# Kernel tuning notes

Hardware: AMD Instinct MI355X
Metric: run time of the kernel (lower is better)

Reference implementation:

```python
import jax, jax.numpy as jnp
import numpy as np

B, G, K = 16, 5000, 256
NUM_CELLS, HID = 100, 64
STEPS, ALPHA = 10, 0.1


def setup_inputs() -> dict:
    key = jax.random.key(0)
    ks = jax.random.split(key, 10)
    ctl = jax.random.normal(ks[0], (B, G), dtype=jnp.float32)
    drug_targets = jax.random.uniform(ks[1], (B, G), dtype=jnp.float32)
    cell_idx = jax.random.randint(ks[2], (B,), 0, NUM_CELLS)
    drug_fp = jax.random.normal(ks[3], (B, 128), dtype=jnp.float32)
    # gene->module membership matrix (constructor constant M_gk)
    M = jax.random.uniform(ks[4], (G, K), dtype=jnp.float32)
    # module-module adjacency (constructor constant A_kk), column-normalized for stability
    A = jax.random.uniform(ks[5], (K, K), dtype=jnp.float32)
    A = A / jnp.sum(A, axis=0, keepdims=True)
    # shared Dense(hidden_dim, relu): input feature dim is 3 (ctl, t, z_gene stacked)
    W1 = jax.random.normal(ks[6], (3, HID), dtype=jnp.float32) * 0.5
    b1 = jnp.zeros((HID,), dtype=jnp.float32)
    cell_emb = jax.random.normal(ks[7], (NUM_CELLS, HID), dtype=jnp.float32) * 0.05
    W2 = jax.random.normal(ks[8], (HID, 1), dtype=jnp.float32) * 0.1
    b2 = jnp.zeros((1,), dtype=jnp.float32)
    return {"ctl": ctl, "drug_targets": drug_targets, "cell_idx": cell_idx,
            "drug_fp": drug_fp, "M": M, "A": A, "W1": W1, "b1": b1,
            "cell_emb": cell_emb, "W2": W2, "b2": b2}


def reference(ctl, drug_targets, cell_idx, drug_fp, M, A, W1, b1, cell_emb, W2, b2):
    t = drug_targets                                   # [B, G]
    # max-pool gene targets into modules: max_g t[b,g] * M[g,k]
    t_mod = jnp.max(t[:, :, None] * M[None, :, :], axis=1)   # [B, K]
    # APPNP propagation: Z = (1-alpha) * Z @ A + alpha * S, fixed 10 steps
    Z = t_mod
    for _ in range(STEPS):
        Z = (1.0 - ALPHA) * (Z @ A) + ALPHA * t_mod
    z_gene = Z @ M.T                                   # [B, G]
    x = jnp.stack([ctl, t, z_gene], axis=-1)           # [B, G, 3]
    h = jax.nn.relu(x @ W1 + b1)                       # [B, G, HID]
    h = h + cell_emb[cell_idx][:, None, :]             # broadcast cell embedding
    y = jnp.squeeze(h @ W2 + b2, axis=-1)              # [B, G]
    return y
```

## Files before the change

kernel.cpp:

```cpp
#include <hip/hip_runtime.h>

#define G 5000
#define K 256
#define BATCH 16
#define HID 64
#define STEPS 10
#define NC 125
#define GPER 40

__global__ void maxpool_kernel(const float* __restrict__ t,
                               const float* __restrict__ M,
                               const float* __restrict__ A,
                               float* __restrict__ partials,
                               float* __restrict__ awarm) {
    __shared__ float tl[GPER][BATCH];
    const int c  = blockIdx.x;
    const int k  = threadIdx.x;
    const int g0 = c * GPER;

    float4 aw = make_float4(0.f, 0.f, 0.f, 0.f);
    if (k < 128)
        aw = ((const float4*)A)[((size_t)blockIdx.x * 128 + k) & 16383];

    for (int i = k; i < GPER * BATCH; i += 256) {
        int gi = i >> 4, b = i & 15;
        tl[gi][b] = t[b * G + g0 + gi];
    }
    __syncthreads();

    float mx[BATCH];
#pragma unroll
    for (int b = 0; b < BATCH; ++b) mx[b] = 0.f;

#pragma unroll 4
    for (int gi = 0; gi < GPER; ++gi) {
        float mg = M[(size_t)(g0 + gi) * K + k];
#pragma unroll
        for (int b = 0; b < BATCH; ++b)
            mx[b] = fmaxf(mx[b], tl[gi][b] * mg);
    }
#pragma unroll
    for (int b = 0; b < BATCH; ++b)
        partials[((size_t)c * BATCH + b) * K + k] = mx[b];

    if (k < 128) awarm[k & 63] = aw.x + aw.y + aw.z + aw.w;
}

__global__ __launch_bounds__(1024, 4)
void appnp_fused(const float* __restrict__ partials,
                 const float* __restrict__ A,
                 const int* __restrict__ cell_idx,
                 const float* __restrict__ cell_emb,
                 const float* __restrict__ W2,
                 const float* __restrict__ b2,
                 float* __restrict__ Zfin,
                 float* __restrict__ ce_dot) {
    __shared__ float4 zb[2][K / 4];
    __shared__ float  Sm[K];
    __shared__ float  red[16][K];
    __shared__ float  ce_red[HID];

    const int b  = blockIdx.x;
    const int t  = threadIdx.x;
    const int k  = t & 255;
    const int jc = t >> 8;
    const int j0 = jc * 64;

    float Areg[64];
#pragma unroll
    for (int jj = 0; jj < 64; ++jj)
        Areg[jj] = A[(size_t)(j0 + jj) * K + k];

    {
        const int k4 = t & 63;
        const int cg = t >> 6;
        const float4* p4 = (const float4*)partials;
        float4 m4 = make_float4(0.f, 0.f, 0.f, 0.f);
        for (int c = cg; c < NC; c += 16) {
            float4 v = p4[((size_t)c * BATCH + b) * (K / 4) + k4];
            m4.x = fmaxf(m4.x, v.x);
            m4.y = fmaxf(m4.y, v.y);
            m4.z = fmaxf(m4.z, v.z);
            m4.w = fmaxf(m4.w, v.w);
        }
        ((float4*)red[cg])[k4] = m4;
    }
    if (t < HID) {
        int ci = cell_idx[b];
        ce_red[t] = cell_emb[ci * HID + t] * W2[t];
    }
    __syncthreads();
    if (jc == 0) {
        float s = red[0][k];
#pragma unroll
        for (int cgi = 1; cgi < 16; ++cgi) s = fmaxf(s, red[cgi][k]);
        Sm[k] = s;
        ((float*)zb)[k] = s;
    }
    if (t == 0) {
        float s = b2[0];
        for (int h = 0; h < HID; ++h) s += ce_red[h];
        ce_dot[b] = s;
    }
    __syncthreads();

    for (int s = 0; s < STEPS; ++s) {
        const float4* cur4 = zb[s & 1] + (j0 >> 2);
        float*        nxt  = (float*)zb[(s + 1) & 1];
        float acc = 0.f;
#pragma unroll
        for (int q = 0; q < 16; ++q) {
            float4 c4 = cur4[q];
            acc = fmaf(c4.x, Areg[4 * q + 0], acc);
            acc = fmaf(c4.y, Areg[4 * q + 1], acc);
            acc = fmaf(c4.z, Areg[4 * q + 2], acc);
            acc = fmaf(c4.w, Areg[4 * q + 3], acc);
        }
        red[jc][k] = acc;
        __syncthreads();
        if (jc == 0)
            nxt[k] = 0.9f * (red[0][k] + red[1][k] + red[2][k] + red[3][k])
                   + 0.1f * Sm[k];
        __syncthreads();
    }
    if (jc == 0) Zfin[b * K + k] = ((float*)zb)[k];
}

__global__ void final_kernel(const float* __restrict__ ctl,
                             const float* __restrict__ t_in,
                             const float* __restrict__ Z,
                             const float* __restrict__ M,
                             const float* __restrict__ W1,
                             const float* __restrict__ b1,
                             const float* __restrict__ W2,
                             const float* __restrict__ ce_dot,
                             float* __restrict__ out) {
    __shared__ float4 zl[BATCH * (K / 4)];
    __shared__ float4 wpack[HID];
    __shared__ float  w2l[HID];
    __shared__ float  cel[BATCH];

    const int t = threadIdx.x;
    const float4* Z4 = (const float4*)Z;
    for (int i = t; i < BATCH * (K / 4); i += 256) zl[i] = Z4[i];
    if (t < HID) {
        wpack[t] = make_float4(W1[t], W1[HID + t], W1[2 * HID + t], b1[t]);
        w2l[t] = W2[t];
    }
    if (t < BATCH) cel[t] = ce_dot[t];
    __syncthreads();

    const int gl = t & 63;
    const int bg = t >> 6;
    const int g = blockIdx.x * 64 + gl;
    if (g >= G) return;

    float acc[4] = {0.f, 0.f, 0.f, 0.f};
    const float4* M4 = (const float4*)(M + (size_t)g * K);
#pragma unroll 4
    for (int k4 = 0; k4 < K / 4; ++k4) {
        float4 m4 = M4[k4];
#pragma unroll
        for (int i = 0; i < 4; ++i) {
            float4 z4 = zl[(bg * 4 + i) * (K / 4) + k4];
            acc[i] = fmaf(m4.x, z4.x, acc[i]);
            acc[i] = fmaf(m4.y, z4.y, acc[i]);
            acc[i] = fmaf(m4.z, z4.z, acc[i]);
            acc[i] = fmaf(m4.w, z4.w, acc[i]);
        }
    }

    float cv[4], tv[4], y[4];
#pragma unroll
    for (int i = 0; i < 4; ++i) {
        int b = bg * 4 + i;
        cv[i] = ctl[b * G + g];
        tv[i] = t_in[b * G + g];
        y[i] = cel[b];
    }
#pragma unroll 4
    for (int h = 0; h < HID; ++h) {
        float4 w = wpack[h];
        float w2h = w2l[h];
#pragma unroll
        for (int i = 0; i < 4; ++i) {
            float pre = w.w;
            pre = fmaf(cv[i], w.x, pre);
            pre = fmaf(tv[i], w.y, pre);
            pre = fmaf(acc[i], w.z, pre);
            pre = fmaxf(pre, 0.f);
            y[i] = fmaf(pre, w2h, y[i]);
        }
    }
#pragma unroll
    for (int i = 0; i < 4; ++i)
        out[(bg * 4 + i) * G + g] = y[i];
}

extern "C" void kernel_launch(void* const* d_in, const int* in_sizes, int n_in,
                              void* d_out, int out_size, void* d_ws, size_t ws_size,
                              hipStream_t stream) {
    const float* ctl      = (const float*)d_in[0];
    const float* tgt      = (const float*)d_in[1];
    const int*   cell_idx = (const int*)d_in[2];
    const float* M        = (const float*)d_in[4];
    const float* A        = (const float*)d_in[5];
    const float* W1       = (const float*)d_in[6];
    const float* b1       = (const float*)d_in[7];
    const float* cell_emb = (const float*)d_in[8];
    const float* W2       = (const float*)d_in[9];
    const float* b2       = (const float*)d_in[10];
    float* out = (float*)d_out;

    float* partials = (float*)d_ws;
    float* Zfin  = partials + (size_t)NC * BATCH * K;
    float* ce    = Zfin + BATCH * K;
    float* awarm = ce + BATCH;

    maxpool_kernel<<<NC, 256, 0, stream>>>(tgt, M, A, partials, awarm);
    appnp_fused<<<BATCH, 1024, 0, stream>>>(partials, A, cell_idx, cell_emb,
                                            W2, b2, Zfin, ce);
    final_kernel<<<(G + 63) / 64, 256, 0, stream>>>(ctl, tgt, Zfin, M, W1, b1,
                                                    W2, ce, out);
}
```

Measured before the change: 114.8 us.

## Split maxpool and final kernels across batch halves to double grid size

The maxpool kernel now splits the K dimension across two blocks and the batch across two thread groups, preloading the 40 M values per thread into registers. The final kernel splits the batch into halves per block, so each thread handles two batch rows instead of four. It also software-prefetches M rows in chunks of eight float4 loads. The aim is more blocks to fill the 256 CUs on MI355X and shorter per-thread dependency chains. The cost is that M is read twice from global or L2 memory in each kernel, plus extra register pressure.

```diff
diff --git a/kernel.cpp b/kernel.cpp
--- a/kernel.cpp
+++ b/kernel.cpp
@@ -8,42 +8,51 @@
 #define NC 125
 #define GPER 40
 
-__global__ void maxpool_kernel(const float* __restrict__ t,
-                               const float* __restrict__ M,
-                               const float* __restrict__ A,
-                               float* __restrict__ partials,
-                               float* __restrict__ awarm) {
+__global__ __launch_bounds__(256)
+void maxpool_kernel(const float* __restrict__ t,
+                    const float* __restrict__ M,
+                    const float* __restrict__ A,
+                    float* __restrict__ partials,
+                    float* __restrict__ awarm) {
     __shared__ float tl[GPER][BATCH];
-    const int c  = blockIdx.x;
-    const int k  = threadIdx.x;
-    const int g0 = c * GPER;
+    const int c   = blockIdx.x >> 1;
+    const int kh  = blockIdx.x & 1;
+    const int tid = threadIdx.x;
+    const int kl  = tid & 127;
+    const int bg  = tid >> 7;
+    const int g0  = c * GPER;
+    const int k   = kh * 128 + kl;
 
     float4 aw = make_float4(0.f, 0.f, 0.f, 0.f);
-    if (k < 128)
-        aw = ((const float4*)A)[((size_t)blockIdx.x * 128 + k) & 16383];
-
-    for (int i = k; i < GPER * BATCH; i += 256) {
+    if (tid < 64)
+        aw = ((const float4*)A)[((size_t)blockIdx.x * 64 + tid) & 16383];
+
+    for (int i = tid; i < GPER * BATCH; i += 256) {
         int gi = i >> 4, b = i & 15;
         tl[gi][b] = t[b * G + g0 + gi];
     }
     __syncthreads();
 
-    float mx[BATCH];
-#pragma unroll
-    for (int b = 0; b < BATCH; ++b) mx[b] = 0.f;
-
-#pragma unroll 4
+    float mrow[GPER];
+#pragma unroll
+    for (int gi = 0; gi < GPER; ++gi)
+        mrow[gi] = M[(size_t)(g0 + gi) * K + k];
+
+    float mx[8];
+#pragma unroll
+    for (int b = 0; b < 8; ++b) mx[b] = 0.f;
+
+#pragma unroll
     for (int gi = 0; gi < GPER; ++gi) {
-        float mg = M[(size_t)(g0 + gi) * K + k];
-#pragma unroll
-        for (int b = 0; b < BATCH; ++b)
-            mx[b] = fmaxf(mx[b], tl[gi][b] * mg);
-    }
-#pragma unroll
-    for (int b = 0; b < BATCH; ++b)
-        partials[((size_t)c * BATCH + b) * K + k] = mx[b];
-
-    if (k < 128) awarm[k & 63] = aw.x + aw.y + aw.z + aw.w;
+#pragma unroll
+        for (int b = 0; b < 8; ++b)
+            mx[b] = fmaxf(mx[b], tl[gi][bg * 8 + b] * mrow[gi]);
+    }
+#pragma unroll
+    for (int b = 0; b < 8; ++b)
+        partials[((size_t)c * BATCH + bg * 8 + b) * K + k] = mx[b];
+
+    if (tid < 64) awarm[tid] = aw.x + aw.y + aw.z + aw.w;
 }
 
 __global__ __launch_bounds__(1024, 4)
@@ -126,75 +135,93 @@
     if (jc == 0) Zfin[b * K + k] = ((float*)zb)[k];
 }
 
-__global__ void final_kernel(const float* __restrict__ ctl,
-                             const float* __restrict__ t_in,
-                             const float* __restrict__ Z,
-                             const float* __restrict__ M,
-                             const float* __restrict__ W1,
-                             const float* __restrict__ b1,
-                             const float* __restrict__ W2,
-                             const float* __restrict__ ce_dot,
-                             float* __restrict__ out) {
-    __shared__ float4 zl[BATCH * (K / 4)];
+__global__ __launch_bounds__(256)
+void final_kernel(const float* __restrict__ ctl,
+                  const float* __restrict__ t_in,
+                  const float* __restrict__ Z,
+                  const float* __restrict__ M,
+                  const float* __restrict__ W1,
+                  const float* __restrict__ b1,
+                  const float* __restrict__ W2,
+                  const float* __restrict__ ce_dot,
+                  float* __restrict__ out) {
+    __shared__ float4 zl[8 * (K / 4)];
     __shared__ float4 wpack[HID];
     __shared__ float  w2l[HID];
-    __shared__ float  cel[BATCH];
-
-    const int t = threadIdx.x;
-    const float4* Z4 = (const float4*)Z;
-    for (int i = t; i < BATCH * (K / 4); i += 256) zl[i] = Z4[i];
-    if (t < HID) {
-        wpack[t] = make_float4(W1[t], W1[HID + t], W1[2 * HID + t], b1[t]);
-        w2l[t] = W2[t];
-    }
-    if (t < BATCH) cel[t] = ce_dot[t];
-    __syncthreads();
-
-    const int gl = t & 63;
-    const int bg = t >> 6;
-    const int g = blockIdx.x * 64 + gl;
+    __shared__ float  cel[8];
+
+    const int tid = threadIdx.x;
+    const int bh  = blockIdx.x & 1;
+    const int gb  = blockIdx.x >> 1;
+    const int b0  = bh * 8;
+
+    const float4* Z4 = (const float4*)Z + (size_t)b0 * (K / 4);
+    for (int i = tid; i < 8 * (K / 4); i += 256) zl[i] = Z4[i];
+    if (tid < HID) {
+        wpack[tid] = make_float4(W1[tid], W1[HID + tid], W1[2 * HID + tid], b1[tid]);
+        w2l[tid] = W2[tid];
+    }
+    if (tid < 8) cel[tid] = ce_dot[b0 + tid];
+    __syncthreads();
+
+    const int gl = tid & 63;
+    const int bg = tid >> 6;
+    const int g  = gb * 64 + gl;
     if (g >= G) return;
 
-    float acc[4] = {0.f, 0.f, 0.f, 0.f};
     const float4* M4 = (const float4*)(M + (size_t)g * K);
-#pragma unroll 4
-    for (int k4 = 0; k4 < K / 4; ++k4) {
-        float4 m4 = M4[k4];
-#pragma unroll
-        for (int i = 0; i < 4; ++i) {
-            float4 z4 = zl[(bg * 4 + i) * (K / 4) + k4];
-            acc[i] = fmaf(m4.x, z4.x, acc[i]);
-            acc[i] = fmaf(m4.y, z4.y, acc[i]);
-            acc[i] = fmaf(m4.z, z4.z, acc[i]);
-            acc[i] = fmaf(m4.w, z4.w, acc[i]);
-        }
-    }
-
-    float cv[4], tv[4], y[4];
-#pragma unroll
-    for (int i = 0; i < 4; ++i) {
-        int b = bg * 4 + i;
-        cv[i] = ctl[b * G + g];
-        tv[i] = t_in[b * G + g];
-        y[i] = cel[b];
-    }
-#pragma unroll 4
+
+    float acc0 = 0.f, acc1 = 0.f;
+    float4 mc[8];
+#pragma unroll
+    for (int u = 0; u < 8; ++u) mc[u] = M4[u];
+
+#pragma unroll
+    for (int kc = 0; kc < 8; ++kc) {
+        float4 mn[8];
+        if (kc < 7) {
+#pragma unroll
+            for (int u = 0; u < 8; ++u) mn[u] = M4[(kc + 1) * 8 + u];
+        }
+#pragma unroll
+        for (int u = 0; u < 8; ++u) {
+            const int k4 = kc * 8 + u;
+            float4 m4 = mc[u];
+            float4 za = zl[(bg * 2 + 0) * (K / 4) + k4];
+            float4 zc = zl[(bg * 2 + 1) * (K / 4) + k4];
+            acc0 = fmaf(m4.x, za.x, acc0);
+            acc0 = fmaf(m4.y, za.y, acc0);
+            acc0 = fmaf(m4.z, za.z, acc0);
+            acc0 = fmaf(m4.w, za.w, acc0);
+            acc1 = fmaf(m4.x, zc.x, acc1);
+            acc1 = fmaf(m4.y, zc.y, acc1);
+            acc1 = fmaf(m4.z, zc.z, acc1);
+            acc1 = fmaf(m4.w, zc.w, acc1);
+        }
+        if (kc < 7) {
+#pragma unroll
+            for (int u = 0; u < 8; ++u) mc[u] = mn[u];
+        }
+    }
+
+    const int ba = b0 + bg * 2;
+    const int bb = ba + 1;
+    float cva = ctl[ba * G + g], cvb = ctl[bb * G + g];
+    float tva = t_in[ba * G + g], tvb = t_in[bb * G + g];
+    float ya  = cel[bg * 2],      yb  = cel[bg * 2 + 1];
+#pragma unroll 8
     for (int h = 0; h < HID; ++h) {
         float4 w = wpack[h];
         float w2h = w2l[h];
-#pragma unroll
-        for (int i = 0; i < 4; ++i) {
-            float pre = w.w;
-            pre = fmaf(cv[i], w.x, pre);
-            pre = fmaf(tv[i], w.y, pre);
-            pre = fmaf(acc[i], w.z, pre);
-            pre = fmaxf(pre, 0.f);
-            y[i] = fmaf(pre, w2h, y[i]);
-        }
-    }
-#pragma unroll
-    for (int i = 0; i < 4; ++i)
-        out[(bg * 4 + i) * G + g] = y[i];
+        float pa = fmaf(cva, w.x, fmaf(tva, w.y, fmaf(acc0, w.z, w.w)));
+        pa = fmaxf(pa, 0.f);
+        ya = fmaf(pa, w2h, ya);
+        float pb = fmaf(cvb, w.x, fmaf(tvb, w.y, fmaf(acc1, w.z, w.w)));
+        pb = fmaxf(pb, 0.f);
+        yb = fmaf(pb, w2h, yb);
+    }
+    out[ba * G + g] = ya;
+    out[bb * G + g] = yb;
 }
 
 extern "C" void kernel_launch(void* const* d_in, const int* in_sizes, int n_in,
@@ -217,9 +244,9 @@
     float* ce    = Zfin + BATCH * K;
     float* awarm = ce + BATCH;
 
-    maxpool_kernel<<<NC, 256, 0, stream>>>(tgt, M, A, partials, awarm);
+    maxpool_kernel<<<NC * 2, 256, 0, stream>>>(tgt, M, A, partials, awarm);
     appnp_fused<<<BATCH, 1024, 0, stream>>>(partials, A, cell_idx, cell_emb,
                                             W2, b2, Zfin, ce);
-    final_kernel<<<(G + 63) / 64, 256, 0, stream>>>(ctl, tgt, Zfin, M, W1, b1,
-                                                    W2, ce, out);
-}
+    final_kernel<<<79 * 2, 256, 0, stream>>>(ctl, tgt, Zfin, M, W1, b1,
+                                             W2, ce, out);
+}
```

Result: faster. 107.2 us (-6.6%).
